# Performance work log

Hardware: AMD Instinct MI355X
Metric: run time of the kernel (lower is better)

## Reference

```python
import jax, jax.numpy as jnp
import numpy as np

B, N, D = 4, 16384, 1024
RANK, NUM_Q = 16, 8
SPARSITY = 0.1
K = max(1, int(N * SPARSITY))  # 1638


def setup_inputs() -> dict:
    key = jax.random.key(0)
    k1, k2, k3 = jax.random.split(key, 3)
    x = jax.random.normal(k1, (B, N, D), dtype=jnp.float32)
    Wk = jax.random.normal(k2, (RANK, D), dtype=jnp.float32)
    queries = jax.random.normal(k3, (NUM_Q, RANK), dtype=jnp.float32)
    return {"x": x, "Wk": Wk, "queries": queries}


def reference(x, Wk, queries):
    # k_proj: [b, n, d] @ [d, rank] -> [b, n, rank]
    keys = jnp.einsum("bnd,rd->bnr", x, Wk)
    # scores: [q, r] x [b, n, r] -> [b, q, n]
    scores = jnp.einsum("qr,bnr->bqn", queries, keys)
    # max over queries -> [b, n]
    token_scores = scores.max(axis=1)
    # eval mode: no jitter noise
    _, indices = jax.lax.top_k(token_scores, K)  # [b, K]
    indices = jnp.sort(indices, axis=-1)
    return indices
```

## Files before the change

kernel.cpp:

```cpp
#include <hip/hip_runtime.h>
#include <stdint.h>

#define B_ 4
#define N_ 16384
#define D_ 1024
#define RANK_ 16
#define NUMQ_ 8
#define KSEL_ 1638

__global__ __launch_bounds__(256) void wq_kernel(const float* __restrict__ Wk,
                                                 const float* __restrict__ queries,
                                                 float* __restrict__ Wq) {
    int i = blockIdx.x * 256 + threadIdx.x;
    if (i >= NUMQ_ * D_) return;
    int q = i >> 10;
    int d = i & (D_ - 1);
    float acc = 0.f;
#pragma unroll
    for (int r = 0; r < RANK_; ++r)
        acc += queries[q * RANK_ + r] * Wk[r * D_ + d];
    Wq[i] = acc;
}

#define TOK 4

#define FOLD(dst, a, b, bit, dist)                          \
    {                                                       \
        float _send = (bit) ? (a) : (b);                    \
        float _recv = __shfl_xor(_send, (dist), 64);        \
        (dst) = ((bit) ? (b) : (a)) + _recv;                \
    }

__global__ __launch_bounds__(256) void score_kernel(const float* __restrict__ x,
                                                    const float* __restrict__ Wq,
                                                    float* __restrict__ scores) {
    __shared__ float sWq[NUMQ_ * D_];
    for (int i = threadIdx.x; i < NUMQ_ * D_; i += 256)
        sWq[i] = Wq[i];
    __syncthreads();

    const int lane = threadIdx.x & 63;
    const int wave = threadIdx.x >> 6;
    const int gw = blockIdx.x * 4 + wave;
    const int numWaves = gridDim.x * 4;
    const int totalTok = B_ * N_;

    const int l5 = (lane >> 5) & 1;
    const int l4 = (lane >> 4) & 1;
    const int l3 = (lane >> 3) & 1;

    for (int t0 = gw * TOK; t0 < totalTok; t0 += numWaves * TOK) {
        float acc[TOK][NUMQ_];
#pragma unroll
        for (int t = 0; t < TOK; ++t)
#pragma unroll
            for (int q = 0; q < NUMQ_; ++q) acc[t][q] = 0.f;

#pragma unroll
        for (int j = 0; j < 4; ++j) {
            const int off = j * 256 + lane * 4;
            float4 xv[TOK];
#pragma unroll
            for (int t = 0; t < TOK; ++t)
                xv[t] = *(const float4*)(x + (size_t)(t0 + t) * D_ + off);
#pragma unroll
            for (int q = 0; q < NUMQ_; ++q) {
                float4 w = *(const float4*)(sWq + q * D_ + off);
#pragma unroll
                for (int t = 0; t < TOK; ++t) {
                    acc[t][q] += xv[t].x * w.x;
                    acc[t][q] += xv[t].y * w.y;
                    acc[t][q] += xv[t].z * w.z;
                    acc[t][q] += xv[t].w * w.w;
                }
            }
        }

#pragma unroll
        for (int t = 0; t < TOK; ++t) {
            float n0, n1, n2, n3;
            FOLD(n0, acc[t][0], acc[t][4], l5, 32)
            FOLD(n1, acc[t][1], acc[t][5], l5, 32)
            FOLD(n2, acc[t][2], acc[t][6], l5, 32)
            FOLD(n3, acc[t][3], acc[t][7], l5, 32)
            float m0, m1;
            FOLD(m0, n0, n2, l4, 16)
            FOLD(m1, n1, n3, l4, 16)
            float p;
            FOLD(p, m0, m1, l3, 8)
            p += __shfl_xor(p, 4, 64);
            p += __shfl_xor(p, 2, 64);
            p += __shfl_xor(p, 1, 64);
            float mx = p;
            mx = fmaxf(mx, __shfl_xor(mx, 8, 64));
            mx = fmaxf(mx, __shfl_xor(mx, 16, 64));
            mx = fmaxf(mx, __shfl_xor(mx, 32, 64));
            if (lane == 0) scores[t0 + t] = mx;
        }
    }
}

__global__ __launch_bounds__(512) void topk_kernel(const float* __restrict__ scores,
                                                   int* __restrict__ out) {
    __shared__ uint32_t sKeys[N_];
    __shared__ uint32_t hist[2048];
    __shared__ uint32_t sSuf[512];
    __shared__ uint32_t waveTot[8];
    __shared__ uint32_t wTotG[8];
    __shared__ int sTs;
    __shared__ uint32_t sPrefix, sR;

    const int b = blockIdx.x;
    const int tid = threadIdx.x;
    const int lane = tid & 63;
    const int wave = tid >> 6;
    const float* s = scores + b * N_;

    for (int i = tid; i < N_; i += 512) {
        uint32_t u = __float_as_uint(s[i]);
        u = (u & 0x80000000u) ? ~u : (u | 0x80000000u);
        sKeys[i] = u;
    }
    __syncthreads();

    uint32_t prefix = 0;
    uint32_t R = KSEL_;

    const int shifts[3] = {21, 10, 0};
    const int widths[3] = {11, 11, 10};

#pragma unroll 1
    for (int pass = 0; pass < 3; ++pass) {
        const int shift = shifts[pass];
        const uint32_t nb = 1u << widths[pass];
        const uint32_t binmask = nb - 1u;
        const uint32_t maskHi = (pass == 0) ? 0u
                              : (0xFFFFFFFFu << (shift + widths[pass]));

        for (int i = tid; i < (int)nb; i += 512) hist[i] = 0;
        __syncthreads();
        for (int i = tid; i < N_; i += 512) {
            uint32_t u = sKeys[i];
            if ((u & maskHi) == prefix)
                atomicAdd(&hist[(u >> shift) & binmask], 1u);
        }
        __syncthreads();

        const int seg = (int)(nb >> 9);
        uint32_t v = 0;
        for (int j = 0; j < seg; ++j) v += hist[tid * seg + j];

#pragma unroll
        for (int d = 1; d < 64; d <<= 1) {
            uint32_t t = __shfl_down(v, (unsigned)d, 64);
            if (lane + d < 64) v += t;
        }
        if (lane == 0) waveTot[wave] = v;
        __syncthreads();
        uint32_t basev = 0;
        for (int w = wave + 1; w < 8; ++w) basev += waveTot[w];
        uint32_t suf = v + basev;
        sSuf[tid] = suf;
        __syncthreads();

        if (suf >= R && (tid == 511 || sSuf[tid + 1] < R)) sTs = tid;
        __syncthreads();
        const int ts = sTs;

        if (tid == 0) {
            uint32_t cum = (ts < 511) ? sSuf[ts + 1] : 0u;
            int sel = ts * seg;
            for (int bin = ts * seg + seg - 1; bin >= ts * seg; --bin) {
                uint32_t c = hist[bin];
                if (cum + c >= R) { sel = bin; break; }
                cum += c;
            }
            sPrefix = prefix | ((uint32_t)sel << shift);
            sR = R - cum;
        }
        __syncthreads();
        prefix = sPrefix;
        R = sR;
        __syncthreads();
    }

    const uint32_t T = prefix;
    const uint32_t need = R;

    const int CHUNK = N_ / 512;
    const int base = tid * CHUNK;
    uint32_t cGT = 0, cEQ = 0;
    for (int i = 0; i < CHUNK; ++i) {
        uint32_t u = sKeys[base + i];
        cGT += (u > T);
        cEQ += (u == T);
    }
    uint32_t packed = (cGT << 16) | cEQ;
    uint32_t pv = packed;
#pragma unroll
    for (int d = 1; d < 64; d <<= 1) {
        uint32_t t = __shfl_up(pv, (unsigned)d, 64);
        if (lane >= d) pv += t;
    }
    if (lane == 63) wTotG[wave] = pv;
    __syncthreads();
    uint32_t pbase = 0;
    for (int w = 0; w < wave; ++w) pbase += wTotG[w];
    uint32_t excl = pbase + pv - packed;
    uint32_t gt = excl >> 16;
    uint32_t eq = excl & 0xFFFFu;

    int* ob = out + b * KSEL_;
    for (int i = 0; i < CHUNK; ++i) {
        uint32_t u = sKeys[base + i];
        if (u > T) {
            uint32_t eqSel = (eq < need) ? eq : need;
            ob[gt + eqSel] = base + i;
            gt++;
        } else if (u == T) {
            if (eq < need) ob[gt + eq] = base + i;
            eq++;
        }
    }
}

extern "C" void kernel_launch(void* const* d_in, const int* in_sizes, int n_in,
                              void* d_out, int out_size, void* d_ws, size_t ws_size,
                              hipStream_t stream) {
    const float* x       = (const float*)d_in[0];
    const float* Wk      = (const float*)d_in[1];
    const float* queries = (const float*)d_in[2];
    int* out = (int*)d_out;

    float* Wq     = (float*)d_ws;
    float* scores = (float*)((char*)d_ws + NUMQ_ * D_ * sizeof(float));

    wq_kernel<<<(NUMQ_ * D_ + 255) / 256, 256, 0, stream>>>(Wk, queries, Wq);
    score_kernel<<<2048, 256, 0, stream>>>(x, Wq, scores);
    topk_kernel<<<B_, 512, 0, stream>>>(scores, out);
}
```

Baseline: 383.9 us.

## Fuse first-pass radix histogram into score kernel and widen top-k block

The score kernel now writes order-preserving uint keys and atomically builds the first radix-pass histogram in global memory, which is zeroed by the Wq kernel. The top-k kernel loads that histogram instead of recomputing pass 0, runs with 1024 threads, and uses vectorized shared-memory reads. The x loads are nontemporal and the Wq staging is vectorized. The aim is to shorten the serial top-k tail, which runs on only four blocks, at the cost of contended global atomics in the score kernel.

```diff
diff --git a/kernel.cpp b/kernel.cpp
--- a/kernel.cpp
+++ b/kernel.cpp
@@ -7,12 +7,17 @@
 #define RANK_ 16
 #define NUMQ_ 8
 #define KSEL_ 1638
+#define NBIN0 2048
+
+typedef float floatx4 __attribute__((ext_vector_type(4)));
 
 __global__ __launch_bounds__(256) void wq_kernel(const float* __restrict__ Wk,
                                                  const float* __restrict__ queries,
-                                                 float* __restrict__ Wq) {
+                                                 float* __restrict__ Wq,
+                                                 unsigned int* __restrict__ ghist) {
     int i = blockIdx.x * 256 + threadIdx.x;
     if (i >= NUMQ_ * D_) return;
+    ghist[i] = 0u;
     int q = i >> 10;
     int d = i & (D_ - 1);
     float acc = 0.f;
@@ -33,10 +38,11 @@
 
 __global__ __launch_bounds__(256) void score_kernel(const float* __restrict__ x,
                                                     const float* __restrict__ Wq,
-                                                    float* __restrict__ scores) {
+                                                    unsigned int* __restrict__ keys,
+                                                    unsigned int* __restrict__ ghist) {
     __shared__ float sWq[NUMQ_ * D_];
-    for (int i = threadIdx.x; i < NUMQ_ * D_; i += 256)
-        sWq[i] = Wq[i];
+    for (int i = threadIdx.x; i < (NUMQ_ * D_) / 4; i += 256)
+        ((float4*)sWq)[i] = ((const float4*)Wq)[i];
     __syncthreads();
 
     const int lane = threadIdx.x & 63;
@@ -59,13 +65,14 @@
 #pragma unroll
         for (int j = 0; j < 4; ++j) {
             const int off = j * 256 + lane * 4;
-            float4 xv[TOK];
+            floatx4 xv[TOK];
 #pragma unroll
             for (int t = 0; t < TOK; ++t)
-                xv[t] = *(const float4*)(x + (size_t)(t0 + t) * D_ + off);
+                xv[t] = __builtin_nontemporal_load(
+                    (const floatx4*)(x + (size_t)(t0 + t) * D_ + off));
 #pragma unroll
             for (int q = 0; q < NUMQ_; ++q) {
-                float4 w = *(const float4*)(sWq + q * D_ + off);
+                floatx4 w = *(const floatx4*)(sWq + q * D_ + off);
 #pragma unroll
                 for (int t = 0; t < TOK; ++t) {
                     acc[t][q] += xv[t].x * w.x;
@@ -76,6 +83,7 @@
             }
         }
 
+        const int bIdx = t0 >> 14;
 #pragma unroll
         for (int t = 0; t < TOK; ++t) {
             float n0, n1, n2, n3;
@@ -95,36 +103,40 @@
             mx = fmaxf(mx, __shfl_xor(mx, 8, 64));
             mx = fmaxf(mx, __shfl_xor(mx, 16, 64));
             mx = fmaxf(mx, __shfl_xor(mx, 32, 64));
-            if (lane == 0) scores[t0 + t] = mx;
-        }
-    }
-}
-
-__global__ __launch_bounds__(512) void topk_kernel(const float* __restrict__ scores,
-                                                   int* __restrict__ out) {
-    __shared__ uint32_t sKeys[N_];
-    __shared__ uint32_t hist[2048];
-    __shared__ uint32_t sSuf[512];
-    __shared__ uint32_t waveTot[8];
-    __shared__ uint32_t wTotG[8];
+            if (lane == t) {
+                unsigned int u = __float_as_uint(mx);
+                u = (u & 0x80000000u) ? ~u : (u | 0x80000000u);
+                keys[t0 + t] = u;
+                atomicAdd(&ghist[bIdx * NBIN0 + (u >> 21)], 1u);
+            }
+        }
+    }
+}
+
+__global__ __launch_bounds__(1024) void topk_kernel(const unsigned int* __restrict__ keys,
+                                                    const unsigned int* __restrict__ ghist,
+                                                    int* __restrict__ out) {
+    __shared__ __align__(16) unsigned int sKeys[N_];
+    __shared__ unsigned int hist[NBIN0];
+    __shared__ unsigned int sSuf[1024];
+    __shared__ unsigned int waveTot[16];
+    __shared__ unsigned int wTotG[16];
     __shared__ int sTs;
-    __shared__ uint32_t sPrefix, sR;
+    __shared__ unsigned int sPrefix, sR;
 
     const int b = blockIdx.x;
     const int tid = threadIdx.x;
     const int lane = tid & 63;
     const int wave = tid >> 6;
-    const float* s = scores + b * N_;
-
-    for (int i = tid; i < N_; i += 512) {
-        uint32_t u = __float_as_uint(s[i]);
-        u = (u & 0x80000000u) ? ~u : (u | 0x80000000u);
-        sKeys[i] = u;
-    }
+
+    const uint4* kv = (const uint4*)(keys + b * N_);
+    uint4* sk4 = (uint4*)sKeys;
+    for (int i = tid; i < N_ / 4; i += 1024) sk4[i] = kv[i];
+    for (int i = tid; i < NBIN0; i += 1024) hist[i] = ghist[b * NBIN0 + i];
     __syncthreads();
 
-    uint32_t prefix = 0;
-    uint32_t R = KSEL_;
+    unsigned int prefix = 0;
+    unsigned int R = KSEL_;
 
     const int shifts[3] = {21, 10, 0};
     const int widths[3] = {11, 11, 10};
@@ -132,50 +144,56 @@
 #pragma unroll 1
     for (int pass = 0; pass < 3; ++pass) {
         const int shift = shifts[pass];
-        const uint32_t nb = 1u << widths[pass];
-        const uint32_t binmask = nb - 1u;
-        const uint32_t maskHi = (pass == 0) ? 0u
-                              : (0xFFFFFFFFu << (shift + widths[pass]));
-
-        for (int i = tid; i < (int)nb; i += 512) hist[i] = 0;
-        __syncthreads();
-        for (int i = tid; i < N_; i += 512) {
-            uint32_t u = sKeys[i];
-            if ((u & maskHi) == prefix)
-                atomicAdd(&hist[(u >> shift) & binmask], 1u);
-        }
-        __syncthreads();
-
-        const int seg = (int)(nb >> 9);
-        uint32_t v = 0;
+        const unsigned int nb = 1u << widths[pass];
+        const unsigned int binmask = nb - 1u;
+
+        if (pass > 0) {
+            const unsigned int maskHi = 0xFFFFFFFFu << (shift + widths[pass]);
+            for (int i = tid; i < (int)nb; i += 1024) hist[i] = 0;
+            __syncthreads();
+            for (int i = tid; i < N_ / 4; i += 1024) {
+                uint4 u4 = sk4[i];
+                unsigned int us[4] = {u4.x, u4.y, u4.z, u4.w};
+#pragma unroll
+                for (int c = 0; c < 4; ++c) {
+                    unsigned int u = us[c];
+                    if ((u & maskHi) == prefix)
+                        atomicAdd(&hist[(u >> shift) & binmask], 1u);
+                }
+            }
+            __syncthreads();
+        }
+
+        const int seg = (int)(nb >> 10);
+        unsigned int v = 0;
         for (int j = 0; j < seg; ++j) v += hist[tid * seg + j];
 
 #pragma unroll
         for (int d = 1; d < 64; d <<= 1) {
-            uint32_t t = __shfl_down(v, (unsigned)d, 64);
+            unsigned int t = __shfl_down(v, (unsigned)d, 64);
             if (lane + d < 64) v += t;
         }
         if (lane == 0) waveTot[wave] = v;
         __syncthreads();
-        uint32_t basev = 0;
-        for (int w = wave + 1; w < 8; ++w) basev += waveTot[w];
-        uint32_t suf = v + basev;
+        unsigned int basev = 0;
+        for (int w = wave + 1; w < 16; ++w) basev += waveTot[w];
+        unsigned int suf = v + basev;
         sSuf[tid] = suf;
         __syncthreads();
 
-        if (suf >= R && (tid == 511 || sSuf[tid + 1] < R)) sTs = tid;
+        if (suf >= R && (tid == 1023 || sSuf[tid + 1] < R)) sTs = tid;
         __syncthreads();
         const int ts = sTs;
 
         if (tid == 0) {
-            uint32_t cum = (ts < 511) ? sSuf[ts + 1] : 0u;
+            unsigned int cum = (ts < 1023) ? sSuf[ts + 1] : 0u;
             int sel = ts * seg;
             for (int bin = ts * seg + seg - 1; bin >= ts * seg; --bin) {
-                uint32_t c = hist[bin];
+                unsigned int c = hist[bin];
                 if (cum + c >= R) { sel = bin; break; }
                 cum += c;
             }
-            sPrefix = prefix | ((uint32_t)sel << shift);
+            sPrefix = prefix | ((unsigned int)sel << shift);
             sR = R - cum;
         }
         __syncthreads();
@@ -184,37 +202,37 @@
         __syncthreads();
     }
 
-    const uint32_t T = prefix;
-    const uint32_t need = R;
-
-    const int CHUNK = N_ / 512;
+    const unsigned int T = prefix;
+    const unsigned int need = R;
+
+    const int CHUNK = N_ / 1024;
     const int base = tid * CHUNK;
-    uint32_t cGT = 0, cEQ = 0;
-    for (int i = 0; i < CHUNK; ++i) {
-        uint32_t u = sKeys[base + i];
-        cGT += (u > T);
-        cEQ += (u == T);
-    }
-    uint32_t packed = (cGT << 16) | cEQ;
-    uint32_t pv = packed;
+    unsigned int cGT = 0, cEQ = 0;
+    for (int i = 0; i < CHUNK / 4; ++i) {
+        uint4 u4 = sk4[(base >> 2) + i];
+        cGT += (u4.x > T) + (u4.y > T) + (u4.z > T) + (u4.w > T);
+        cEQ += (u4.x == T) + (u4.y == T) + (u4.z == T) + (u4.w == T);
+    }
+    unsigned int packed = (cGT << 16) | cEQ;
+    unsigned int pv = packed;
 #pragma unroll
     for (int d = 1; d < 64; d <<= 1) {
-        uint32_t t = __shfl_up(pv, (unsigned)d, 64);
+        unsigned int t = __shfl_up(pv, (unsigned)d, 64);
         if (lane >= d) pv += t;
     }
     if (lane == 63) wTotG[wave] = pv;
     __syncthreads();
-    uint32_t pbase = 0;
+    unsigned int pbase = 0;
     for (int w = 0; w < wave; ++w) pbase += wTotG[w];
-    uint32_t excl = pbase + pv - packed;
-    uint32_t gt = excl >> 16;
-    uint32_t eq = excl & 0xFFFFu;
+    unsigned int excl = pbase + pv - packed;
+    unsigned int gt = excl >> 16;
+    unsigned int eq = excl & 0xFFFFu;
 
     int* ob = out + b * KSEL_;
     for (int i = 0; i < CHUNK; ++i) {
-        uint32_t u = sKeys[base + i];
+        unsigned int u = sKeys[base + i];
         if (u > T) {
-            uint32_t eqSel = (eq < need) ? eq : need;
+            unsigned int eqSel = (eq < need) ? eq : need;
             ob[gt + eqSel] = base + i;
             gt++;
         } else if (u == T) {
@@ -232,10 +250,11 @@
     const float* queries = (const float*)d_in[2];
     int* out = (int*)d_out;
 
-    float* Wq     = (float*)d_ws;
-    float* scores = (float*)((char*)d_ws + NUMQ_ * D_ * sizeof(float));
-
-    wq_kernel<<<(NUMQ_ * D_ + 255) / 256, 256, 0, stream>>>(Wk, queries, Wq);
-    score_kernel<<<2048, 256, 0, stream>>>(x, Wq, scores);
-    topk_kernel<<<B_, 512, 0, stream>>>(scores, out);
-}
+    float*        Wq    = (float*)d_ws;
+    unsigned int* keys  = (unsigned int*)((char*)d_ws + 32 * 1024);
+    unsigned int* ghist = (unsigned int*)((char*)d_ws + (32 + 256) * 1024);
+
+    wq_kernel<<<(NUMQ_ * D_ + 255) / 256, 256, 0, stream>>>(Wk, queries, Wq, ghist);
+    score_kernel<<<2048, 256, 0, stream>>>(x, Wq, keys, ghist);
+    topk_kernel<<<B_, 1024, 0, stream>>>(keys, ghist, out);
+}
```

Result: slower. 638.0 us (+66.2%).
